# Kernel optimization log

Measured on AMD Instinct MI355X. Metric: run time of the kernel, lower is better.

The kernel has to match this reference:

```python
import jax, jax.numpy as jnp
import numpy as np

BN_EPS = 1e-5


def _maxpool2(x):
    # x: [b, c, h, w] -> [b, c, h//2, w//2], 2x2 max pool, stride 2
    b, c, h, w = x.shape
    return x.reshape(b, c, h // 2, 2, w // 2, 2).max(axis=(3, 5))


def setup_inputs() -> dict:
    key = jax.random.key(0)
    ks = jax.random.split(key, 9)
    b, C, H, W = 8, 512, 64, 64
    Ci = C // 2  # inter_channels = 256
    return {
        "x": jax.random.normal(ks[0], (b, C, H, W), dtype=jnp.float32),
        "g_w": jax.random.normal(ks[1], (Ci, C), dtype=jnp.float32) * 0.02,
        "g_b": jax.random.normal(ks[2], (Ci,), dtype=jnp.float32) * 0.02,
        "W_w": jax.random.normal(ks[3], (C, Ci), dtype=jnp.float32) * 0.02,
        "W_b": jax.random.normal(ks[4], (C,), dtype=jnp.float32) * 0.02,
        "bn_gamma": jax.random.normal(ks[5], (C,), dtype=jnp.float32),
        "bn_beta": jax.random.normal(ks[6], (C,), dtype=jnp.float32),
        "bn_mean": jax.random.normal(ks[7], (C,), dtype=jnp.float32),
        "bn_var": jax.random.uniform(ks[8], (C,), dtype=jnp.float32, minval=0.5, maxval=1.5),
    }


def reference(x, g_w, g_b, W_w, W_b, bn_gamma, bn_beta, bn_mean, bn_var):
    b, C, H, W = x.shape
    Ci = g_w.shape[0]

    # g branch: conv1x1 (C -> Ci) then 2x2 maxpool, flatten to values [b, Nk, Ci]
    g_x = jnp.einsum('bchw,oc->bohw', x, g_w) + g_b[None, :, None, None]
    g_x = _maxpool2(g_x).reshape(b, Ci, -1).transpose(0, 2, 1)  # [b, Nk, Ci]

    # theta: identity, flattened queries [b, Nq, C]
    theta = x.reshape(b, C, -1).transpose(0, 2, 1)  # [b, Nq, C]
    # phi: identity + 2x2 maxpool, keys [b, C, Nk]
    phi = _maxpool2(x).reshape(b, C, -1)  # [b, C, Nk]

    # attention (unscaled dot product + softmax over keys)
    f = jnp.einsum('bnc,bck->bnk', theta, phi)  # [b, Nq, Nk]
    attn = jax.nn.softmax(f, axis=-1)
    y = jnp.einsum('bnk,bko->bno', attn, g_x)  # [b, Nq, Ci]
    y = y.transpose(0, 2, 1).reshape(b, Ci, H, W)

    # W: conv1x1 (Ci -> C) + BatchNorm2d (eval mode with running stats)
    W_y = jnp.einsum('bchw,oc->bohw', y, W_w) + W_b[None, :, None, None]
    inv_std = jax.lax.rsqrt(bn_var + BN_EPS)
    W_y = (W_y - bn_mean[None, :, None, None]) * (bn_gamma * inv_std)[None, :, None, None] \
          + bn_beta[None, :, None, None]

    return W_y + x
```

## Files before the change

### kernel.cpp

```cpp
#include <hip/hip_runtime.h>
#include <stdint.h>

typedef __attribute__((ext_vector_type(4))) float f32x4;
typedef __attribute__((ext_vector_type(8))) short short8_t;
typedef __attribute__((ext_vector_type(8))) unsigned short ushort8_t;

__device__ __forceinline__ unsigned short f2bf(float f) {
    unsigned int u = __builtin_bit_cast(unsigned int, f);
    u = (u + 0x7fffu + ((u >> 16) & 1u)) >> 16;
    return (unsigned short)u;
}
__device__ __forceinline__ float bf2f(unsigned short h) {
    unsigned int u = ((unsigned int)h) << 16;
    return __builtin_bit_cast(float, u);
}

__device__ __forceinline__ void gll16(const unsigned short* g, unsigned short* l) {
    __builtin_amdgcn_global_load_lds(
        (const __attribute__((address_space(1))) void*)g,
        (__attribute__((address_space(3))) void*)l, 16, 0, 0);
}

__global__ __launch_bounds__(256) void prep_w(
    const float* __restrict__ g_w, const float* __restrict__ W_w,
    const float* __restrict__ W_b, const float* __restrict__ gamma,
    const float* __restrict__ beta, const float* __restrict__ mean,
    const float* __restrict__ var,
    unsigned short* __restrict__ gwb, unsigned short* __restrict__ wwb,
    float* __restrict__ bnA, float* __restrict__ bnB)
{
    int i = blockIdx.x * 256 + threadIdx.x;
    if (i < 256 * 512) { gwb[i] = f2bf(g_w[i]); wwb[i] = f2bf(W_w[i]); }
    if (i < 512) {
        float is = rsqrtf(var[i] + 1e-5f);
        float a = gamma[i] * is;
        bnA[i] = a;
        bnB[i] = (W_b[i] - mean[i]) * a + beta[i];
    }
}

__global__ __launch_bounds__(256) void build_qk(
    const float* __restrict__ x, unsigned short* __restrict__ Qh,
    unsigned short* __restrict__ Kh)
{
    __shared__ float t[32][129];
    int b = blockIdx.z;
    int p0 = blockIdx.x * 128, c0 = blockIdx.y * 32;
    const float* xb = x + (long)b * 512 * 4096;
    int tid = threadIdx.x;
    for (int i = 0; i < 16; i++) {
        int idx = i * 256 + tid;
        int c = idx >> 7, p = idx & 127;
        t[c][p] = xb[(long)(c0 + c) * 4096 + p0 + p];
    }
    __syncthreads();
    unsigned short* qb = Qh + (long)b * 4096 * 512;
    for (int i = 0; i < 16; i++) {
        int idx = i * 256 + tid;
        int p = idx >> 5, c = idx & 31;
        qb[(long)(p0 + p) * 512 + c0 + c] = f2bf(t[c][p]);
    }
    unsigned short* kb = Kh + (long)b * 1024 * 512;
    int kp0 = p0 >> 2;
    for (int i = 0; i < 4; i++) {
        int idx = i * 256 + tid;
        int w = idx >> 5, c = idx & 31;
        float v = fmaxf(fmaxf(t[c][2 * w], t[c][2 * w + 1]),
                        fmaxf(t[c][64 + 2 * w], t[c][64 + 2 * w + 1]));
        kb[(long)(kp0 + w) * 512 + c0 + c] = f2bf(v);
    }
}

__global__ __launch_bounds__(256) void build_v(
    const unsigned short* __restrict__ Gt, const float* __restrict__ g_b,
    unsigned short* __restrict__ Gp)
{
    int b = blockIdx.z;
    int k  = blockIdx.x * 32 + (threadIdx.x & 31);
    int ci = blockIdx.y * 8 + (threadIdx.x >> 5);
    int h = k >> 5, w = k & 31;
    const unsigned short* g = Gt + (long)b * 4096 * 256;
    long p = (long)(h * 128 + w * 2) * 256 + ci;
    float v0 = bf2f(g[p]),        v1 = bf2f(g[p + 256]);
    float v2 = bf2f(g[p + 64*256]), v3 = bf2f(g[p + 65*256]);
    float v = fmaxf(fmaxf(v0, v1), fmaxf(v2, v3)) + g_b[ci];
    Gp[(long)b * 256 * 1024 + (long)ci * 1024 + k] = f2bf(v);
}

__global__ __launch_bounds__(256) void smax_rows(
    const unsigned short* __restrict__ S, float* __restrict__ Smax)
{
    long row = (long)blockIdx.x * 4 + (threadIdx.x >> 6);
    int lane = threadIdx.x & 63;
    const unsigned short* r = S + row * 1024 + lane * 16;
    ushort8_t v0 = *(const ushort8_t*)r;
    ushort8_t v1 = *(const ushort8_t*)(r + 8);
    float m = -3.0e38f;
    for (int e = 0; e < 8; e++) m = fmaxf(m, fmaxf(bf2f(v0[e]), bf2f(v1[e])));
    for (int off = 32; off; off >>= 1) m = fmaxf(m, __shfl_xor(m, off));
    if (lane == 0) Smax[row] = m;
}

__global__ __launch_bounds__(256) void pv_fused(
    const unsigned short* __restrict__ S, long sbstr,
    const float* __restrict__ Smax, long mxstr,
    const unsigned short* __restrict__ Gp, long gbstr,
    unsigned short* __restrict__ Y, long ybstr)
{
    __shared__ unsigned short lV[256 * 64];
    __shared__ unsigned short lP[64 * 64];
    __shared__ float li[64];

    const int tid = threadIdx.x;
    const int wid = tid >> 6, lane = tid & 63;

    unsigned gx = gridDim.x, gy = gridDim.y;
    unsigned nwg = gx * gy;
    unsigned lin = blockIdx.x + gx * blockIdx.y;
    unsigned l = ((nwg & 7u) == 0u) ? ((lin & 7u) * (nwg >> 3) + (lin >> 3)) : lin;
    unsigned bx = l % gx, by = l / gx;

    const int q0 = (int)bx * 64;
    const unsigned short* Sb = S + by * sbstr + (long)q0 * 1024;
    const unsigned short* Gb = Gp + by * gbstr;
    unsigned short* Yb = Y + by * ybstr + (long)q0 * 256;

    const int wr = wid >> 1, wc = wid & 1;
    const int lr = lane & 15, lg = lane >> 4;
    const int srA = lane >> 3;
    const int scg = (((lane & 7) ^ srA) << 3);
    const int pr = tid >> 2;
    const int pc = (tid & 3) * 2;

    const float m = Smax[by * mxstr + q0 + pr];

    f32x4 acc[2][8];
    for (int mi = 0; mi < 2; mi++)
        for (int ni = 0; ni < 8; ni++)
            acc[mi][ni] = (f32x4){0.f, 0.f, 0.f, 0.f};
    float psum = 0.f;

    for (int kb = 0; kb < 16; kb++) {
        __syncthreads();
        const unsigned short* sp = Sb + (long)pr * 1024 + kb * 64 + pc * 8;
        ushort8_t v0 = *(const ushort8_t*)sp;
        ushort8_t v1 = *(const ushort8_t*)(sp + 8);
        for (int i = 0; i < 8; i++) {
            int cibase = i * 32 + wid * 8;
            gll16(Gb + (long)(cibase + srA) * 1024 + kb * 64 + scg, &lV[cibase * 64]);
        }
        {
            ushort8_t o8;
            for (int e = 0; e < 8; e++) {
                float pe = __expf(bf2f(v0[e]) - m);
                psum += pe;
                o8[e] = f2bf(pe);
            }
            *(ushort8_t*)(&lP[pr * 64 + ((pc ^ (pr & 7)) * 8)]) = o8;
            for (int e = 0; e < 8; e++) {
                float pe = __expf(bf2f(v1[e]) - m);
                psum += pe;
                o8[e] = f2bf(pe);
            }
            *(ushort8_t*)(&lP[pr * 64 + (((pc + 1) ^ (pr & 7)) * 8)]) = o8;
        }
        __syncthreads();
        for (int ks = 0; ks < 2; ks++) {
            short8_t af[2], bfr[8];
            for (int mi = 0; mi < 2; mi++) {
                int row = wr * 32 + mi * 16 + lr;
                int ch = ((ks * 4 + lg) ^ (row & 7)) * 8;
                af[mi] = *(const short8_t*)(&lP[row * 64 + ch]);
            }
            for (int ni = 0; ni < 8; ni++) {
                int row = wc * 128 + ni * 16 + lr;
                int ch = ((ks * 4 + lg) ^ (row & 7)) * 8;
                bfr[ni] = *(const short8_t*)(&lV[row * 64 + ch]);
            }
            for (int mi = 0; mi < 2; mi++)
                for (int ni = 0; ni < 8; ni++)
                    acc[mi][ni] = __builtin_amdgcn_mfma_f32_16x16x32_bf16(
                        af[mi], bfr[ni], acc[mi][ni], 0, 0, 0);
        }
    }

    psum += __shfl_xor(psum, 1);
    psum += __shfl_xor(psum, 2);
    if ((tid & 3) == 0) li[pr] = 1.0f / psum;
    __syncthreads();

    for (int mi = 0; mi < 2; mi++) {
        for (int ni = 0; ni < 8; ni++) {
            int ci = wc * 128 + ni * 16 + lr;
            int rbase = wr * 32 + mi * 16 + lg * 4;
            for (int r = 0; r < 4; r++) {
                int row = rbase + r;
                Yb[(long)row * 256 + ci] = f2bf(acc[mi][ni][r] * li[row]);
            }
        }
    }
}

__global__ __launch_bounds__(256) void gemm_qkg(
    const unsigned short* __restrict__ Qh,
    const unsigned short* __restrict__ Kh,
    const unsigned short* __restrict__ gwb,
    unsigned short* __restrict__ S,
    unsigned short* __restrict__ Gt)
{
    __shared__ unsigned short lA[128 * 64];
    __shared__ unsigned short lB[128 * 64];
    const int tid = threadIdx.x;
    const int wid = tid >> 6, lane = tid & 63;

    unsigned gx = gridDim.x, gy = gridDim.y;
    unsigned nwg = gx * gy * gridDim.z;
    unsigned lin = blockIdx.x + gx * (blockIdx.y + gy * blockIdx.z);
    unsigned l = ((nwg & 7u) == 0u) ? ((lin & 7u) * (nwg >> 3) + (lin >> 3)) : lin;
    unsigned bx = l % gx;
    unsigned rem = l / gx;
    unsigned by = rem % gy;
    unsigned bz = rem / gy;

    const int z = (int)bz;
    const int m0 = (int)by * 128;
    const unsigned short* Ab = Qh + (long)z * 4096 * 512;
    const unsigned short* Bb;
    unsigned short* Cb;
    int n0, ldc;
    if (bx < 8) {
        Bb = Kh + (long)z * 1024 * 512;  n0 = bx * 128;
        Cb = S + (long)z * 4096 * 1024;  ldc = 1024;
    } else {
        Bb = gwb;                         n0 = (bx - 8) * 128;
        Cb = Gt + (long)z * 4096 * 256;   ldc = 256;
    }

    const int wr = wid >> 1, wc = wid & 1;
    const int lr = lane & 15, lg = lane >> 4;
    const int srA = lane >> 3;
    const int scg = (((lane & 7) ^ srA) << 3);

    f32x4 acc[4][4];
    for (int mi = 0; mi < 4; mi++)
        for (int ni = 0; ni < 4; ni++)
            acc[mi][ni] = (f32x4){0.f, 0.f, 0.f, 0.f};

    for (int k0 = 0; k0 < 512; k0 += 64) {
        __syncthreads();
        for (int i = 0; i < 4; i++) {
            int rowbase = i * 32 + wid * 8;
            gll16(Ab + (long)(m0 + rowbase + srA) * 512 + k0 + scg, &lA[rowbase * 64]);
            gll16(Bb + (long)(n0 + rowbase + srA) * 512 + k0 + scg, &lB[rowbase * 64]);
        }
        __syncthreads();
        for (int kk = 0; kk < 2; kk++) {
            short8_t af[4], bfr[4];
            for (int mi = 0; mi < 4; mi++) {
                int row = wr * 64 + mi * 16 + lr;
                int ch = ((kk * 4 + lg) ^ (row & 7)) * 8;
                af[mi] = *(const short8_t*)(&lA[row * 64 + ch]);
            }
            for (int ni = 0; ni < 4; ni++) {
                int row = wc * 64 + ni * 16 + lr;
                int ch = ((kk * 4 + lg) ^ (row & 7)) * 8;
                bfr[ni] = *(const short8_t*)(&lB[row * 64 + ch]);
            }
            for (int mi = 0; mi < 4; mi++)
                for (int ni = 0; ni < 4; ni++)
                    acc[mi][ni] = __builtin_amdgcn_mfma_f32_16x16x32_bf16(
                        af[mi], bfr[ni], acc[mi][ni], 0, 0, 0);
        }
    }

    for (int mi = 0; mi < 4; mi++) {
        for (int ni = 0; ni < 4; ni++) {
            int ncol = n0 + wc * 64 + ni * 16 + lr;
            int mrow = m0 + wr * 64 + mi * 16 + lg * 4;
            for (int r = 0; r < 4; r++) {
                Cb[(long)(mrow + r) * ldc + ncol] = f2bf(acc[mi][ni][r]);
            }
        }
    }
}

template<int EPI>
__global__ __launch_bounds__(256) void gemm_abt(
    const unsigned short* __restrict__ A, int lda, long abstr,
    const unsigned short* __restrict__ B, int ldb, long bbstr,
    void* __restrict__ Cv, int ldc, long cbstr,
    int K,
    const float* __restrict__ bnA, const float* __restrict__ bnB,
    const float* __restrict__ Xres, long xbstr)
{
    __shared__ unsigned short lA[128 * 64];
    __shared__ unsigned short lB[128 * 64];
    const int tid = threadIdx.x;
    const int wid = tid >> 6, lane = tid & 63;

    unsigned gx = gridDim.x, gy = gridDim.y;
    unsigned nwg = gx * gy * gridDim.z;
    unsigned lin = blockIdx.x + gx * (blockIdx.y + gy * blockIdx.z);
    unsigned l = ((nwg & 7u) == 0u) ? ((lin & 7u) * (nwg >> 3) + (lin >> 3)) : lin;
    unsigned bx = l % gx;
    unsigned rem = l / gx;
    unsigned by = rem % gy;
    unsigned bz = rem / gy;

    const int z = (int)bz;
    const int m0 = (int)by * 128, n0 = (int)bx * 128;
    const unsigned short* Ab = A + z * abstr;
    const unsigned short* Bb = B + z * bbstr;
    const int wr = wid >> 1, wc = wid & 1;
    const int lr = lane & 15, lg = lane >> 4;

    const int srA = lane >> 3;
    const int scg = (((lane & 7) ^ srA) << 3);

    f32x4 acc[4][4];
    for (int mi = 0; mi < 4; mi++)
        for (int ni = 0; ni < 4; ni++)
            acc[mi][ni] = (f32x4){0.f, 0.f, 0.f, 0.f};

    for (int k0 = 0; k0 < K; k0 += 64) {
        __syncthreads();
        for (int i = 0; i < 4; i++) {
            int rowbase = i * 32 + wid * 8;
            gll16(Ab + (long)(m0 + rowbase + srA) * lda + k0 + scg, &lA[rowbase * 64]);
            gll16(Bb + (long)(n0 + rowbase + srA) * ldb + k0 + scg, &lB[rowbase * 64]);
        }
        __syncthreads();
        for (int kk = 0; kk < 2; kk++) {
            short8_t af[4], bfr[4];
            for (int mi = 0; mi < 4; mi++) {
                int row = wr * 64 + mi * 16 + lr;
                int ch = ((kk * 4 + lg) ^ (row & 7)) * 8;
                af[mi] = *(const short8_t*)(&lA[row * 64 + ch]);
            }
            for (int ni = 0; ni < 4; ni++) {
                int row = wc * 64 + ni * 16 + lr;
                int ch = ((kk * 4 + lg) ^ (row & 7)) * 8;
                bfr[ni] = *(const short8_t*)(&lB[row * 64 + ch]);
            }
            for (int mi = 0; mi < 4; mi++)
                for (int ni = 0; ni < 4; ni++)
                    acc[mi][ni] = __builtin_amdgcn_mfma_f32_16x16x32_bf16(
                        af[mi], bfr[ni], acc[mi][ni], 0, 0, 0);
        }
    }

    for (int mi = 0; mi < 4; mi++) {
        for (int ni = 0; ni < 4; ni++) {
            int ncol = n0 + wc * 64 + ni * 16 + lr;
            int mrow = m0 + wr * 64 + mi * 16 + lg * 4;
            for (int r = 0; r < 4; r++) {
                int row = mrow + r;
                float v = acc[mi][ni][r];
                long idx = z * cbstr + (long)row * ldc + ncol;
                if (EPI == 0) {
                    ((float*)Cv)[idx] = v;
                } else if (EPI == 1) {
                    ((unsigned short*)Cv)[idx] = f2bf(v);
                } else {
                    float o = v * bnA[row] + bnB[row] + Xres[z * xbstr + (long)row * ldc + ncol];
                    ((float*)Cv)[idx] = o;
                }
            }
        }
    }
}

__global__ void copy_residual(const float* __restrict__ x, float* __restrict__ out, long n)
{
    for (long i = blockIdx.x * 256ll + threadIdx.x; i < n; i += (long)gridDim.x * 256)
        out[i] = x[i];
}

extern "C" void kernel_launch(void* const* d_in, const int* in_sizes, int n_in,
                              void* d_out, int out_size, void* d_ws, size_t ws_size,
                              hipStream_t stream)
{
    const float* x     = (const float*)d_in[0];
    const float* g_w   = (const float*)d_in[1];
    const float* g_b   = (const float*)d_in[2];
    const float* W_w   = (const float*)d_in[3];
    const float* W_b   = (const float*)d_in[4];
    const float* gamma = (const float*)d_in[5];
    const float* beta  = (const float*)d_in[6];
    const float* mean  = (const float*)d_in[7];
    const float* var   = (const float*)d_in[8];
    float* out = (float*)d_out;

    char* ws = (char*)d_ws;
    size_t o = 0;
    auto alloc = [&](size_t bytes) { size_t r = o; o = (o + bytes + 255) & ~(size_t)255; return r; };
    size_t o_gwb = alloc(256 * 512 * 2);
    size_t o_wwb = alloc(512 * 256 * 2);
    size_t o_bnA = alloc(512 * 4);
    size_t o_bnB = alloc(512 * 4);
    size_t o_q   = alloc(8ull * 4096 * 512 * 2);
    size_t o_k   = alloc(8ull * 1024 * 512 * 2);
    size_t o_gp  = alloc(8ull * 256 * 1024 * 2);
    size_t o_y   = alloc(8ull * 4096 * 256 * 2);
    size_t o_m   = alloc(8ull * 4096 * 4);
    size_t o_s   = o;
    const size_t srow_bytes = 1024ull * 2;
    const size_t sb1 = 4096ull * srow_bytes;

    int G = 0, RC = 0;
    if      (o_s + 8 * sb1 <= ws_size) G = 8;
    else if (o_s + 4 * sb1 <= ws_size) G = 4;
    else if (o_s + 2 * sb1 <= ws_size) G = 2;
    else if (o_s + 1 * sb1 <= ws_size) G = 1;
    else {
        for (int rc = 2048; rc >= 128; rc >>= 1)
            if (o_s + (size_t)rc * srow_bytes <= ws_size) { RC = rc; break; }
        if (!RC) {
            copy_residual<<<dim3(2048), dim3(256), 0, stream>>>(x, out, (long)out_size);
            return;
        }
    }

    unsigned short* gwb = (unsigned short*)(ws + o_gwb);
    unsigned short* wwb = (unsigned short*)(ws + o_wwb);
    float* bnA = (float*)(ws + o_bnA);
    float* bnB = (float*)(ws + o_bnB);
    unsigned short* Qh  = (unsigned short*)(ws + o_q);
    unsigned short* Kh  = (unsigned short*)(ws + o_k);
    unsigned short* Gp  = (unsigned short*)(ws + o_gp);
    unsigned short* Y   = (unsigned short*)(ws + o_y);
    float* Smax         = (float*)(ws + o_m);
    unsigned short* S   = (unsigned short*)(ws + o_s);

    prep_w<<<dim3(512), dim3(256), 0, stream>>>(g_w, W_w, W_b, gamma, beta, mean, var,
                                                gwb, wwb, bnA, bnB);
    build_qk<<<dim3(32, 16, 8), dim3(256), 0, stream>>>(x, Qh, Kh);

    if (G) {
        for (int bg = 0; bg < 8; bg += G) {
            gemm_qkg<<<dim3(10, 32, G), dim3(256), 0, stream>>>(
                Qh + (size_t)bg * 4096 * 512,
                Kh + (size_t)bg * 1024 * 512,
                gwb,
                S,
                Y + (size_t)bg * 4096 * 256);
            build_v<<<dim3(32, 32, G), dim3(256), 0, stream>>>(
                Y + (size_t)bg * 4096 * 256, g_b, Gp + (size_t)bg * 256 * 1024);
            smax_rows<<<dim3(G * 1024), dim3(256), 0, stream>>>(S, Smax);
            pv_fused<<<dim3(64, G), dim3(256), 0, stream>>>(
                S, 4096l * 1024,
                Smax, 4096,
                Gp + (size_t)bg * 256 * 1024, 256l * 1024,
                Y + (size_t)bg * 4096 * 256, 4096l * 256);
        }
    } else {
        gemm_abt<1><<<dim3(2, 32, 8), dim3(256), 0, stream>>>(
            Qh, 512, 4096l * 512,
            gwb, 512, 0,
            (void*)Y, 256, 4096l * 256, 512,
            nullptr, nullptr, nullptr, 0);
        build_v<<<dim3(32, 32, 8), dim3(256), 0, stream>>>(Y, g_b, Gp);
        for (int b = 0; b < 8; b++) {
            for (int r0 = 0; r0 < 4096; r0 += RC) {
                const unsigned short* Aq = Qh + (size_t)b * 4096 * 512 + (size_t)r0 * 512;
                gemm_abt<1><<<dim3(8, RC / 128, 1), dim3(256), 0, stream>>>(
                    Aq, 512, 0,
                    Kh + (size_t)b * 1024 * 512, 512, 0,
                    (void*)S, 1024, 0, 512,
                    nullptr, nullptr, nullptr, 0);
                smax_rows<<<dim3(RC / 4), dim3(256), 0, stream>>>(S, Smax);
                pv_fused<<<dim3(RC / 64, 1), dim3(256), 0, stream>>>(
                    S, 0,
                    Smax, 0,
                    Gp + (size_t)b * 256 * 1024, 0,
                    Y + ((size_t)b * 4096 + r0) * 256, 0);
            }
        }
    }

    gemm_abt<2><<<dim3(32, 4, 8), dim3(256), 0, stream>>>(
        wwb, 256, 0,
        Y, 256, 4096l * 256,
        (void*)out, 4096, 512l * 4096, 256,
        bnA, bnB, x, 512l * 4096);
}
```

Measured before the change: 174.6 us.

## Fuse row-max into PV kernel and vectorize Q/K construction stores

Removes the separate smax_rows kernel and its global Smax buffer. Each pv_fused block now computes the row maxima of its 64 score rows into shared memory before the main loop, which saves a kernel launch and a global write/read round trip. The cost is an extra serial prologue per block that reads the S rows twice (once for the max, once for PV). Separately, build_qk now uses float4 loads and 8-wide bf16 vector stores instead of scalar accesses.

```diff
diff --git a/kernel.cpp b/kernel.cpp
--- a/kernel.cpp
+++ b/kernel.cpp
@@ -48,26 +48,33 @@
     int p0 = blockIdx.x * 128, c0 = blockIdx.y * 32;
     const float* xb = x + (long)b * 512 * 4096;
     int tid = threadIdx.x;
-    for (int i = 0; i < 16; i++) {
-        int idx = i * 256 + tid;
-        int c = idx >> 7, p = idx & 127;
-        t[c][p] = xb[(long)(c0 + c) * 4096 + p0 + p];
+    for (int i = 0; i < 4; i++) {
+        int f4 = i * 256 + tid;
+        int c = f4 >> 5, p4 = (f4 & 31) * 4;
+        float4 v = *(const float4*)(xb + (long)(c0 + c) * 4096 + p0 + p4);
+        t[c][p4] = v.x; t[c][p4 + 1] = v.y; t[c][p4 + 2] = v.z; t[c][p4 + 3] = v.w;
     }
     __syncthreads();
     unsigned short* qb = Qh + (long)b * 4096 * 512;
-    for (int i = 0; i < 16; i++) {
-        int idx = i * 256 + tid;
-        int p = idx >> 5, c = idx & 31;
-        qb[(long)(p0 + p) * 512 + c0 + c] = f2bf(t[c][p]);
+    for (int i = 0; i < 2; i++) {
+        int u = i * 256 + tid;
+        int p = u >> 2, cg = (u & 3) * 8;
+        ushort8_t o;
+        for (int e = 0; e < 8; e++) o[e] = f2bf(t[cg + e][p]);
+        *(ushort8_t*)(qb + (long)(p0 + p) * 512 + c0 + cg) = o;
     }
     unsigned short* kb = Kh + (long)b * 1024 * 512;
     int kp0 = p0 >> 2;
-    for (int i = 0; i < 4; i++) {
-        int idx = i * 256 + tid;
-        int w = idx >> 5, c = idx & 31;
-        float v = fmaxf(fmaxf(t[c][2 * w], t[c][2 * w + 1]),
-                        fmaxf(t[c][64 + 2 * w], t[c][64 + 2 * w + 1]));
-        kb[(long)(kp0 + w) * 512 + c0 + c] = f2bf(v);
+    if (tid < 128) {
+        int w = tid >> 2, cg = (tid & 3) * 8;
+        ushort8_t o;
+        for (int e = 0; e < 8; e++) {
+            int c = cg + e;
+            float v = fmaxf(fmaxf(t[c][2 * w], t[c][2 * w + 1]),
+                            fmaxf(t[c][64 + 2 * w], t[c][64 + 2 * w + 1]));
+            o[e] = f2bf(v);
+        }
+        *(ushort8_t*)(kb + (long)(kp0 + w) * 512 + c0 + cg) = o;
     }
 }
 
@@ -87,29 +94,14 @@
     Gp[(long)b * 256 * 1024 + (long)ci * 1024 + k] = f2bf(v);
 }
 
-__global__ __launch_bounds__(256) void smax_rows(
-    const unsigned short* __restrict__ S, float* __restrict__ Smax)
-{
-    long row = (long)blockIdx.x * 4 + (threadIdx.x >> 6);
-    int lane = threadIdx.x & 63;
-    const unsigned short* r = S + row * 1024 + lane * 16;
-    ushort8_t v0 = *(const ushort8_t*)r;
-    ushort8_t v1 = *(const ushort8_t*)(r + 8);
-    float m = -3.0e38f;
-    for (int e = 0; e < 8; e++) m = fmaxf(m, fmaxf(bf2f(v0[e]), bf2f(v1[e])));
-    for (int off = 32; off; off >>= 1) m = fmaxf(m, __shfl_xor(m, off));
-    if (lane == 0) Smax[row] = m;
-}
-
 __global__ __launch_bounds__(256) void pv_fused(
     const unsigned short* __restrict__ S, long sbstr,
-    const float* __restrict__ Smax, long mxstr,
     const unsigned short* __restrict__ Gp, long gbstr,
     unsigned short* __restrict__ Y, long ybstr)
 {
     __shared__ unsigned short lV[256 * 64];
     __shared__ unsigned short lP[64 * 64];
-    __shared__ float li[64];
+    __shared__ float lm[64], li[64];
 
     const int tid = threadIdx.x;
     const int wid = tid >> 6, lane = tid & 63;
@@ -124,6 +116,19 @@
     const unsigned short* Sb = S + by * sbstr + (long)q0 * 1024;
     const unsigned short* Gb = Gp + by * gbstr;
     unsigned short* Yb = Y + by * ybstr + (long)q0 * 256;
+
+    for (int rr = 0; rr < 16; rr++) {
+        int r = (wid << 4) + rr;
+        const unsigned short* pS = Sb + (long)r * 1024 + lane * 16;
+        ushort8_t v0 = *(const ushort8_t*)pS;
+        ushort8_t v1 = *(const ushort8_t*)(pS + 8);
+        float m = -3.0e38f;
+        for (int e = 0; e < 8; e++)
+            m = fmaxf(m, fmaxf(bf2f(v0[e]), bf2f(v1[e])));
+        for (int off = 32; off; off >>= 1) m = fmaxf(m, __shfl_xor(m, off));
+        if (lane == 0) lm[r] = m;
+    }
+    __syncthreads();
 
     const int wr = wid >> 1, wc = wid & 1;
     const int lr = lane & 15, lg = lane >> 4;
@@ -132,7 +137,7 @@
     const int pr = tid >> 2;
     const int pc = (tid & 3) * 2;
 
-    const float m = Smax[by * mxstr + q0 + pr];
+    const float m = lm[pr];
 
     f32x4 acc[2][8];
     for (int mi = 0; mi < 2; mi++)
@@ -402,7 +407,6 @@
     size_t o_k   = alloc(8ull * 1024 * 512 * 2);
     size_t o_gp  = alloc(8ull * 256 * 1024 * 2);
     size_t o_y   = alloc(8ull * 4096 * 256 * 2);
-    size_t o_m   = alloc(8ull * 4096 * 4);
     size_t o_s   = o;
     const size_t srow_bytes = 1024ull * 2;
     const size_t sb1 = 4096ull * srow_bytes;
@@ -429,7 +433,6 @@
     unsigned short* Kh  = (unsigned short*)(ws + o_k);
     unsigned short* Gp  = (unsigned short*)(ws + o_gp);
     unsigned short* Y   = (unsigned short*)(ws + o_y);
-    float* Smax         = (float*)(ws + o_m);
     unsigned short* S   = (unsigned short*)(ws + o_s);
 
     prep_w<<<dim3(512), dim3(256), 0, stream>>>(g_w, W_w, W_b, gamma, beta, mean, var,
@@ -446,10 +449,8 @@
                 Y + (size_t)bg * 4096 * 256);
             build_v<<<dim3(32, 32, G), dim3(256), 0, stream>>>(
                 Y + (size_t)bg * 4096 * 256, g_b, Gp + (size_t)bg * 256 * 1024);
-            smax_rows<<<dim3(G * 1024), dim3(256), 0, stream>>>(S, Smax);
             pv_fused<<<dim3(64, G), dim3(256), 0, stream>>>(
                 S, 4096l * 1024,
-                Smax, 4096,
                 Gp + (size_t)bg * 256 * 1024, 256l * 1024,
                 Y + (size_t)bg * 4096 * 256, 4096l * 256);
         }
@@ -468,10 +469,8 @@
                     Kh + (size_t)b * 1024 * 512, 512, 0,
                     (void*)S, 1024, 0, 512,
                     nullptr, nullptr, nullptr, 0);
-                smax_rows<<<dim3(RC / 4), dim3(256), 0, stream>>>(S, Smax);
                 pv_fused<<<dim3(RC / 64, 1), dim3(256), 0, stream>>>(
                     S, 0,
-                    Smax, 0,
                     Gp + (size_t)b * 256 * 1024, 0,
                     Y + ((size_t)b * 4096 + r0) * 256, 0);
             }
```

Result: no change. 171.8 us (-1.6%).
